# Kernel optimization log

Hardware: AMD Instinct MI355X
Metric: run time of the kernel (lower is better)

Reference implementation:

```python
import jax, jax.numpy as jnp
import numpy as np

N = 50000      # n_nodes
E = 800000     # n_edges (avg degree 16)
D_IN, D_HID, D_OUT = 128, 128, 64


def setup_inputs() -> dict:
    key = jax.random.key(0)
    k1, k2, k3, k4 = jax.random.split(key, 4)
    x = jax.random.normal(k1, (N, D_IN), jnp.float32)
    edge_index = jax.random.randint(k2, (2, E), 0, N, jnp.int32)
    # Glorot-style init for the two GCNConv linear weights
    W1 = jax.random.normal(k3, (D_IN, D_HID), jnp.float32) / np.sqrt(D_IN)
    W2 = jax.random.normal(k4, (D_HID, D_OUT), jnp.float32) / np.sqrt(D_HID)
    b1 = jnp.zeros((D_HID,), jnp.float32)
    b2 = jnp.zeros((D_OUT,), jnp.float32)
    return {"x": x, "edge_index": edge_index, "W1": W1, "b1": b1, "W2": W2, "b2": b2}


def _gcn_conv(x, W, b, src, dst):
    """PyG GCNConv: linear transform, then sym-normalized aggregation with self-loops."""
    h = x @ W                                   # [N, F_out]
    ones = jnp.ones((src.shape[0],), h.dtype)
    # degree includes the self-loop weight of 1
    deg = jax.ops.segment_sum(ones, dst, num_segments=N) + 1.0
    dinv = jax.lax.rsqrt(deg)                   # D^{-1/2}
    norm = dinv[src] * dinv[dst]                # per-edge normalization
    agg = jax.ops.segment_sum(h[src] * norm[:, None], dst, num_segments=N)
    # self-loop contribution: norm_ii = dinv_i^2
    return agg + h * (dinv * dinv)[:, None] + b


def reference(x, edge_index, W1, b1, W2, b2):
    src, dst = edge_index[0], edge_index[1]
    h = jax.nn.relu(_gcn_conv(x, W1, b1, src, dst))
    out = jax.nn.relu(_gcn_conv(h, W2, b2, src, dst))
    return out
```

## Files before the change

kernel.cpp:

```cpp
#include <hip/hip_runtime.h>

typedef unsigned short u16;
typedef __attribute__((ext_vector_type(8))) short short8;
typedef __attribute__((ext_vector_type(4))) float f32x4;

__device__ __forceinline__ float bflo(unsigned u) {
    union { unsigned u; float f; } v; v.u = u << 16; return v.f;
}
__device__ __forceinline__ float bfhi(unsigned u) {
    union { unsigned u; float f; } v; v.u = u & 0xFFFF0000u; return v.f;
}
__device__ __forceinline__ float bf2f(u16 h) {
    union { unsigned u; float f; } v; v.u = ((unsigned)h) << 16; return v.f;
}
__device__ __forceinline__ u16 f2bf(float f) {
    union { float f; unsigned u; } v; v.f = f;
    unsigned u = v.u;
    u += 0x7FFFu + ((u >> 16) & 1u);
    return (u16)(u >> 16);
}

__global__ void k_detect(const u16* __restrict__ x, int* __restrict__ flag) {
    __shared__ int c_s;
    if (threadIdx.x == 0) c_s = 0;
    __syncthreads();
    int c = 0;
    for (int i = threadIdx.x; i < 2048; i += blockDim.x) {
        int e = (x[2 * i] >> 7) & 0xFF;
        c += (e >= 160 || e <= 80) ? 1 : 0;
    }
    atomicAdd(&c_s, c);
    __syncthreads();
    if (threadIdx.x == 0) *flag = (c_s > 64) ? 1 : 0;
}

__global__ void k_convert_w(const void* __restrict__ W1, const void* __restrict__ b1,
                            const void* __restrict__ W2, const void* __restrict__ b2,
                            u16* __restrict__ out, const int* __restrict__ flag) {
    const int n1 = 128 * 128, n2 = n1 + 128, n3 = n2 + 128 * 64, n4 = n3 + 64;
    int i = blockIdx.x * 256 + threadIdx.x;
    if (i >= n4) return;
    const void* src; int off;
    if (i < n1)      { src = W1; off = i; }
    else if (i < n2) { src = b1; off = i - n1; }
    else if (i < n3) { src = W2; off = i - n2; }
    else             { src = b2; off = i - n3; }
    out[i] = *flag ? f2bf(((const float*)src)[off]) : ((const u16*)src)[off];
}


__global__ void k_degpos(const int* __restrict__ dst, int* __restrict__ cnt,
                         int* __restrict__ pos, int E) {
    int e = blockIdx.x * blockDim.x + threadIdx.x;
    if (e < E) pos[e] = atomicAdd(&cnt[dst[e]], 1);
}

__global__ void k_scan_blocks(const int* __restrict__ cnt, int* __restrict__ rowp,
                              int* __restrict__ sums, int n) {
    __shared__ int s[256];
    int t = threadIdx.x;
    int i = blockIdx.x * 256 + t;
    int v = (i < n) ? cnt[i] : 0;
    s[t] = v;
    __syncthreads();
    for (int off = 1; off < 256; off <<= 1) {
        int add = (t >= off) ? s[t - off] : 0;
        __syncthreads();
        s[t] += add;
        __syncthreads();
    }
    if (i < n) rowp[i] = s[t] - v;
    if (t == 255) sums[blockIdx.x] = s[255];
}

__global__ void k_finalize2(int* __restrict__ rowp, const int* __restrict__ sums,
                            const int* __restrict__ cnt, float* __restrict__ dinv,
                            int n, int E) {
    __shared__ int s[256];
    int t = threadIdx.x;
    int b = blockIdx.x;
    s[t] = sums[t];
    __syncthreads();
    for (int off = 1; off < 256; off <<= 1) {
        int add = (t >= off) ? s[t - off] : 0;
        __syncthreads();
        s[t] += add;
        __syncthreads();
    }
    int prefix = (b == 0) ? 0 : s[b - 1];
    int i = b * 256 + t;
    if (i < n) {
        rowp[i] += prefix;
        dinv[i] = rsqrtf((float)cnt[i] + 1.0f);
    }
    if (i == 0) rowp[n] = E;
}


__global__ void k_gemm1_fill(const void* __restrict__ Av, const u16* __restrict__ W,
                             const float* __restrict__ dinv, u16* __restrict__ out,
                             int M, int GB, const int* __restrict__ flag,
                             const int* __restrict__ src, const int* __restrict__ dst,
                             const int* __restrict__ pos, const int* __restrict__ rowp,
                             int* __restrict__ col, int E) {
    constexpr int NOUT = 128;
    int t = threadIdx.x;
    if ((int)blockIdx.x >= GB) {
        int stride = (gridDim.x - GB) * 256;
        for (int e = ((int)blockIdx.x - GB) * 256 + t; e < E; e += stride)
            col[rowp[dst[e]] + pos[e]] = src[e];
        return;
    }
    __shared__ u16 Wt[NOUT][136];
    for (int idx = t; idx < NOUT * 128; idx += 256) {
        int k = idx / NOUT, n = idx % NOUT;
        Wt[n][k] = W[idx];
    }
    __syncthreads();
    int wave = t >> 6, lane = t & 63;
    int m0 = ((int)blockIdx.x * 4 + wave) * 16;
    if (m0 >= M) return;
    int q = lane >> 4;
    int mr = lane & 15;

    short8 a[4];
    if (*flag) {
        const float* arow = (const float*)Av + (size_t)(m0 + mr) * 128 + q * 8;
#pragma unroll
        for (int c = 0; c < 4; c++) {
            f32x4 lo = *(const f32x4*)(arow + c * 32);
            f32x4 hi = *(const f32x4*)(arow + c * 32 + 4);
            a[c][0] = (short)f2bf(lo.x); a[c][1] = (short)f2bf(lo.y);
            a[c][2] = (short)f2bf(lo.z); a[c][3] = (short)f2bf(lo.w);
            a[c][4] = (short)f2bf(hi.x); a[c][5] = (short)f2bf(hi.y);
            a[c][6] = (short)f2bf(hi.z); a[c][7] = (short)f2bf(hi.w);
        }
    } else {
        const u16* arow = (const u16*)Av + (size_t)(m0 + mr) * 128 + q * 8;
#pragma unroll
        for (int c = 0; c < 4; c++) a[c] = *(const short8*)(arow + c * 32);
    }

    f32x4 acc[NOUT / 16];
#pragma unroll
    for (int tl = 0; tl < NOUT / 16; tl++) acc[tl] = (f32x4){0.f, 0.f, 0.f, 0.f};
#pragma unroll
    for (int c = 0; c < 4; c++) {
#pragma unroll
        for (int tl = 0; tl < NOUT / 16; tl++) {
            short8 b = *(const short8*)(&Wt[tl * 16 + mr][c * 32 + q * 8]);
            acc[tl] = __builtin_amdgcn_mfma_f32_16x16x32_bf16(a[c], b, acc[tl], 0, 0, 0);
        }
    }
    int rbase = m0 + q * 4;
#pragma unroll
    for (int tl = 0; tl < NOUT / 16; tl++) {
#pragma unroll
        for (int r = 0; r < 4; r++) {
            int row = rbase + r;
            float v = acc[tl][r] * dinv[row];
            out[(size_t)row * NOUT + tl * 16 + mr] = f2bf(v);
        }
    }
}


template <int NOUT>
__global__ void k_gemm_scale(const u16* __restrict__ A, const u16* __restrict__ W,
                             const float* __restrict__ dinv, u16* __restrict__ out, int M) {
    __shared__ u16 Wt[NOUT][136];
    int t = threadIdx.x;
    for (int idx = t; idx < NOUT * 128; idx += 256) {
        int k = idx / NOUT, n = idx % NOUT;
        Wt[n][k] = W[idx];
    }
    __syncthreads();
    int wave = t >> 6, lane = t & 63;
    int m0 = ((int)blockIdx.x * 4 + wave) * 16;
    if (m0 >= M) return;
    int q = lane >> 4;
    int mr = lane & 15;

    const u16* arow = A + (size_t)(m0 + mr) * 128 + q * 8;
    short8 a[4];
#pragma unroll
    for (int c = 0; c < 4; c++) a[c] = *(const short8*)(arow + c * 32);

    f32x4 acc[NOUT / 16];
#pragma unroll
    for (int tl = 0; tl < NOUT / 16; tl++) acc[tl] = (f32x4){0.f, 0.f, 0.f, 0.f};
#pragma unroll
    for (int c = 0; c < 4; c++) {
#pragma unroll
        for (int tl = 0; tl < NOUT / 16; tl++) {
            short8 b = *(const short8*)(&Wt[tl * 16 + mr][c * 32 + q * 8]);
            acc[tl] = __builtin_amdgcn_mfma_f32_16x16x32_bf16(a[c], b, acc[tl], 0, 0, 0);
        }
    }
    int rbase = m0 + q * 4;
#pragma unroll
    for (int tl = 0; tl < NOUT / 16; tl++) {
#pragma unroll
        for (int r = 0; r < 4; r++) {
            int row = rbase + r;
            float v = acc[tl][r] * dinv[row];
            out[(size_t)row * NOUT + tl * 16 + mr] = f2bf(v);
        }
    }
}


template <int F>
__global__ void k_agg(const u16* __restrict__ g, const int* __restrict__ rowp,
                      const int* __restrict__ col, const float* __restrict__ dinv,
                      const u16* __restrict__ bias, u16* __restrict__ outh,
                      float* __restrict__ outf, const int* __restrict__ flag,
                      int N, int E) {
    constexpr int LPR = F / 8;
    constexpr int EPW = 64 / LPR;
    int d = blockIdx.x * 4 + (threadIdx.x >> 6);
    if (d >= N) return;
    int lane = threadIdx.x & 63;
    int er = lane / LPR;
    int fo = (lane % LPR) * 8;

    int beg = rowp[d], end = rowp[d + 1];
    if (beg < 0) beg = 0;
    if (end > E) end = E;
    int deg = end - beg;

    float a0[8], a1[8];
#pragma unroll
    for (int j = 0; j < 8; j++) { a0[j] = 0.f; a1[j] = 0.f; }

    for (int base = 0; base < deg; base += 64) {
        int cnt = deg - base; if (cnt > 64) cnt = 64;
        int colv = 0;
        if (lane < cnt) {
            int s = col[beg + base + lane];
            colv = s < 0 ? 0 : (s >= N ? N - 1 : s);
        }
        int full = cnt / EPW;
        int i = 0;
        for (; i + 2 <= full; i += 2) {
            int s0 = __shfl(colv, i * EPW + er, 64);
            int s1 = __shfl(colv, (i + 1) * EPW + er, 64);
            uint4 v0 = *(const uint4*)(g + (size_t)s0 * F + fo);
            uint4 v1 = *(const uint4*)(g + (size_t)s1 * F + fo);
            a0[0] += bflo(v0.x); a0[1] += bfhi(v0.x);
            a0[2] += bflo(v0.y); a0[3] += bfhi(v0.y);
            a0[4] += bflo(v0.z); a0[5] += bfhi(v0.z);
            a0[6] += bflo(v0.w); a0[7] += bfhi(v0.w);
            a1[0] += bflo(v1.x); a1[1] += bfhi(v1.x);
            a1[2] += bflo(v1.y); a1[3] += bfhi(v1.y);
            a1[4] += bflo(v1.z); a1[5] += bfhi(v1.z);
            a1[6] += bflo(v1.w); a1[7] += bfhi(v1.w);
        }
        if (i < full) {
            int s0 = __shfl(colv, i * EPW + er, 64);
            uint4 v0 = *(const uint4*)(g + (size_t)s0 * F + fo);
            a0[0] += bflo(v0.x); a0[1] += bfhi(v0.x);
            a0[2] += bflo(v0.y); a0[3] += bfhi(v0.y);
            a0[4] += bflo(v0.z); a0[5] += bfhi(v0.z);
            a0[6] += bflo(v0.w); a0[7] += bfhi(v0.w);
            i++;
        }
        int rem = cnt - full * EPW;
        int s0 = __shfl(colv, (full * EPW + er) & 63, 64);
        if (er < rem) {
            uint4 v0 = *(const uint4*)(g + (size_t)s0 * F + fo);
            a0[0] += bflo(v0.x); a0[1] += bfhi(v0.x);
            a0[2] += bflo(v0.y); a0[3] += bfhi(v0.y);
            a0[4] += bflo(v0.z); a0[5] += bfhi(v0.z);
            a0[6] += bflo(v0.w); a0[7] += bfhi(v0.w);
        }
    }
#pragma unroll
    for (int j = 0; j < 8; j++) a0[j] += a1[j];
#pragma unroll
    for (int off = LPR; off < 64; off <<= 1) {
#pragma unroll
        for (int j = 0; j < 8; j++) a0[j] += __shfl_xor(a0[j], off, 64);
    }

    if (lane < LPR) {
        uint4 sv = *(const uint4*)(g + (size_t)d * F + fo);
        uint4 bv = *(const uint4*)(bias + fo);
        float di = dinv[d];
        float r[8];
        r[0] = di * (a0[0] + bflo(sv.x)) + bflo(bv.x);
        r[1] = di * (a0[1] + bfhi(sv.x)) + bfhi(bv.x);
        r[2] = di * (a0[2] + bflo(sv.y)) + bflo(bv.y);
        r[3] = di * (a0[3] + bfhi(sv.y)) + bfhi(bv.y);
        r[4] = di * (a0[4] + bflo(sv.z)) + bflo(bv.z);
        r[5] = di * (a0[5] + bfhi(sv.z)) + bfhi(bv.z);
        r[6] = di * (a0[6] + bflo(sv.w)) + bflo(bv.w);
        r[7] = di * (a0[7] + bfhi(sv.w)) + bfhi(bv.w);
#pragma unroll
        for (int j = 0; j < 8; j++) r[j] = r[j] > 0.f ? r[j] : 0.f;
        size_t o = (size_t)d * F + fo;
        if (flag && *flag) {
            f32x4 w0 = {r[0], r[1], r[2], r[3]};
            f32x4 w1 = {r[4], r[5], r[6], r[7]};
            *(f32x4*)(outf + o) = w0;
            *(f32x4*)(outf + o + 4) = w1;
        } else {
            uint4 w;
            w.x = (unsigned)f2bf(r[0]) | ((unsigned)f2bf(r[1]) << 16);
            w.y = (unsigned)f2bf(r[2]) | ((unsigned)f2bf(r[3]) << 16);
            w.z = (unsigned)f2bf(r[4]) | ((unsigned)f2bf(r[5]) << 16);
            w.w = (unsigned)f2bf(r[6]) | ((unsigned)f2bf(r[7]) << 16);
            *(uint4*)(outh + o) = w;
        }
    }
}


extern "C" void kernel_launch(void* const* d_in, const int* in_sizes, int n_in,
                              void* d_out, int out_size, void* d_ws, size_t ws_size,
                              hipStream_t stream) {
    const int N = in_sizes[0] / 128;
    const int E = in_sizes[1] / 2;
    const int* ei = (const int*)d_in[1];
    const int* src = ei;
    const int* dst = ei + E;

    char* p = (char*)d_ws;
    auto alloc = [&](size_t b) { char* r = p; p += (b + 255) & ~(size_t)255; return r; };
    int*   flag = (int*)alloc(256);
    int*   rowp = (int*)alloc((size_t)(N + 1) * 4);
    float* dinv = (float*)alloc((size_t)N * 4);
    int*   col  = (int*)alloc((size_t)E * 4);
    u16*   wbuf = (u16*)alloc((size_t)(128 * 128 + 128 + 128 * 64 + 64) * 2);
    char*  slotA = alloc((size_t)N * 128 * 2);
    char*  slotB = alloc((size_t)N * 128 * 2);

    int* cnt  = (int*)slotA;
    int* sums = (int*)(slotA + (size_t)N * 4);
    u16* g1   = (u16*)slotA;
    u16* g2   = (u16*)slotA;
    int* pos  = (int*)slotB;
    u16* o1   = (u16*)slotB;
    u16* W1C = wbuf;
    u16* b1C = wbuf + 128 * 128;
    u16* W2C = b1C + 128;
    u16* b2C = W2C + 128 * 64;

    k_detect<<<1, 256, 0, stream>>>((const u16*)d_in[0], flag);
    k_convert_w<<<97, 256, 0, stream>>>(d_in[2], d_in[3], d_in[4], d_in[5], wbuf, flag);

    hipMemsetAsync(slotA, 0, (size_t)N * 4 + 1024, stream);
    int eb = (E + 255) / 256;
    int nb = (N + 255) / 256;
    k_degpos<<<eb, 256, 0, stream>>>(dst, cnt, pos, E);
    k_scan_blocks<<<nb, 256, 0, stream>>>(cnt, rowp, sums, N);
    k_finalize2<<<nb, 256, 0, stream>>>(rowp, sums, cnt, dinv, N, E);

    int GB = (N / 16 + 3) / 4;
    int FB = GB;
    k_gemm1_fill<<<GB + FB, 256, 0, stream>>>(d_in[0], W1C, dinv, g1, N, GB, flag,
                                              src, dst, pos, rowp, col, E);

    int ab = (N + 3) / 4;
    k_agg<128><<<ab, 256, 0, stream>>>(g1, rowp, col, dinv, b1C,
                                       o1, nullptr, nullptr, N, E);
    k_gemm_scale<64><<<GB, 256, 0, stream>>>(o1, W2C, dinv, g2, N);
    k_agg<64><<<ab, 256, 0, stream>>>(g2, rowp, col, dinv, b2C,
                                      (u16*)d_out, (float*)d_out, flag, N, E);
}
```

Measured before the change: 214.3 us.

## Fold dtype detection and weight conversion into consumers, merge scan kernels

The dtype-detect kernel is merged into the degree-count kernel as block 0. The separate weight/bias conversion kernel is removed, and each GEMM or aggregation kernel now converts fp32 weights and biases on the fly while loading them into shared memory or registers. The two-pass block scan is collapsed into one kernel in which every block recomputes all block sums from the counts with vectorised loads. The intent is to drop three launches and a small memset region, at the cost of redundant per-block sum work and per-block weight conversion.

```diff
diff --git a/kernel.cpp b/kernel.cpp
--- a/kernel.cpp
+++ b/kernel.cpp
@@ -9,9 +9,6 @@
 }
 __device__ __forceinline__ float bfhi(unsigned u) {
     union { unsigned u; float f; } v; v.u = u & 0xFFFF0000u; return v.f;
-}
-__device__ __forceinline__ float bf2f(u16 h) {
-    union { unsigned u; float f; } v; v.u = ((unsigned)h) << 16; return v.f;
 }
 __device__ __forceinline__ u16 f2bf(float f) {
     union { float f; unsigned u; } v; v.f = f;
@@ -20,84 +17,65 @@
     return (u16)(u >> 16);
 }
 
-__global__ void k_detect(const u16* __restrict__ x, int* __restrict__ flag) {
-    __shared__ int c_s;
-    if (threadIdx.x == 0) c_s = 0;
-    __syncthreads();
-    int c = 0;
-    for (int i = threadIdx.x; i < 2048; i += blockDim.x) {
-        int e = (x[2 * i] >> 7) & 0xFF;
-        c += (e >= 160 || e <= 80) ? 1 : 0;
-    }
-    atomicAdd(&c_s, c);
-    __syncthreads();
-    if (threadIdx.x == 0) *flag = (c_s > 64) ? 1 : 0;
-}
-
-__global__ void k_convert_w(const void* __restrict__ W1, const void* __restrict__ b1,
-                            const void* __restrict__ W2, const void* __restrict__ b2,
-                            u16* __restrict__ out, const int* __restrict__ flag) {
-    const int n1 = 128 * 128, n2 = n1 + 128, n3 = n2 + 128 * 64, n4 = n3 + 64;
-    int i = blockIdx.x * 256 + threadIdx.x;
-    if (i >= n4) return;
-    const void* src; int off;
-    if (i < n1)      { src = W1; off = i; }
-    else if (i < n2) { src = b1; off = i - n1; }
-    else if (i < n3) { src = W2; off = i - n2; }
-    else             { src = b2; off = i - n3; }
-    out[i] = *flag ? f2bf(((const float*)src)[off]) : ((const u16*)src)[off];
-}
-
-
-__global__ void k_degpos(const int* __restrict__ dst, int* __restrict__ cnt,
-                         int* __restrict__ pos, int E) {
-    int e = blockIdx.x * blockDim.x + threadIdx.x;
+__global__ void k_deg_detect(const int* __restrict__ dst, int* __restrict__ cnt,
+                             int* __restrict__ pos, int E,
+                             const u16* __restrict__ x, int* __restrict__ flag) {
+    if (blockIdx.x == 0) {
+        __shared__ int c_s;
+        if (threadIdx.x == 0) c_s = 0;
+        __syncthreads();
+        int c = 0;
+        for (int i = threadIdx.x; i < 2048; i += 256) {
+            int ex = (x[2 * i] >> 7) & 0xFF;
+            c += (ex >= 160 || ex <= 80) ? 1 : 0;
+        }
+        atomicAdd(&c_s, c);
+        __syncthreads();
+        if (threadIdx.x == 0) *flag = (c_s > 64) ? 1 : 0;
+    }
+    int e = blockIdx.x * 256 + threadIdx.x;
     if (e < E) pos[e] = atomicAdd(&cnt[dst[e]], 1);
 }
 
-__global__ void k_scan_blocks(const int* __restrict__ cnt, int* __restrict__ rowp,
-                              int* __restrict__ sums, int n) {
-    __shared__ int s[256];
+__global__ void k_scan(const int* __restrict__ cnt, int* __restrict__ rowp,
+                       float* __restrict__ dinv, int n, int E, int nb) {
+    __shared__ int S[256];
+    __shared__ int T[256];
     int t = threadIdx.x;
-    int i = blockIdx.x * 256 + t;
-    int v = (i < n) ? cnt[i] : 0;
-    s[t] = v;
+    int b = blockIdx.x;
+    int s = 0;
+    if (t < nb) {
+        const int4* p4 = (const int4*)(cnt + t * 256);
+#pragma unroll 8
+        for (int i = 0; i < 64; i++) { int4 v = p4[i]; s += v.x + v.y + v.z + v.w; }
+    }
+    S[t] = s;
     __syncthreads();
     for (int off = 1; off < 256; off <<= 1) {
-        int add = (t >= off) ? s[t - off] : 0;
-        __syncthreads();
-        s[t] += add;
-        __syncthreads();
-    }
-    if (i < n) rowp[i] = s[t] - v;
-    if (t == 255) sums[blockIdx.x] = s[255];
-}
-
-__global__ void k_finalize2(int* __restrict__ rowp, const int* __restrict__ sums,
-                            const int* __restrict__ cnt, float* __restrict__ dinv,
-                            int n, int E) {
-    __shared__ int s[256];
-    int t = threadIdx.x;
-    int b = blockIdx.x;
-    s[t] = sums[t];
+        int add = (t >= off) ? S[t - off] : 0;
+        __syncthreads();
+        S[t] += add;
+        __syncthreads();
+    }
+    int prefix = (b == 0) ? 0 : S[b - 1];
+    int i = b * 256 + t;
+    int v = (i < n) ? cnt[i] : 0;
+    T[t] = v;
     __syncthreads();
     for (int off = 1; off < 256; off <<= 1) {
-        int add = (t >= off) ? s[t - off] : 0;
-        __syncthreads();
-        s[t] += add;
-        __syncthreads();
-    }
-    int prefix = (b == 0) ? 0 : s[b - 1];
-    int i = b * 256 + t;
+        int add = (t >= off) ? T[t - off] : 0;
+        __syncthreads();
+        T[t] += add;
+        __syncthreads();
+    }
     if (i < n) {
-        rowp[i] += prefix;
-        dinv[i] = rsqrtf((float)cnt[i] + 1.0f);
+        rowp[i] = prefix + T[t] - v;
+        dinv[i] = rsqrtf((float)v + 1.0f);
     }
     if (i == 0) rowp[n] = E;
 }
 
-
-__global__ void k_gemm1_fill(const void* __restrict__ Av, const u16* __restrict__ W,
+__global__ void k_gemm1_fill(const void* __restrict__ Av, const void* __restrict__ W,
                              const float* __restrict__ dinv, u16* __restrict__ out,
                              int M, int GB, const int* __restrict__ flag,
                              const int* __restrict__ src, const int* __restrict__ dst,
@@ -111,10 +89,11 @@
             col[rowp[dst[e]] + pos[e]] = src[e];
         return;
     }
+    int fl = *flag;
     __shared__ u16 Wt[NOUT][136];
     for (int idx = t; idx < NOUT * 128; idx += 256) {
         int k = idx / NOUT, n = idx % NOUT;
-        Wt[n][k] = W[idx];
+        Wt[n][k] = fl ? f2bf(((const float*)W)[idx]) : ((const u16*)W)[idx];
     }
     __syncthreads();
     int wave = t >> 6, lane = t & 63;
@@ -124,7 +103,7 @@
     int mr = lane & 15;
 
     short8 a[4];
-    if (*flag) {
+    if (fl) {
         const float* arow = (const float*)Av + (size_t)(m0 + mr) * 128 + q * 8;
 #pragma unroll
         for (int c = 0; c < 4; c++) {
@@ -164,15 +143,16 @@
     }
 }
 
-
 template <int NOUT>
-__global__ void k_gemm_scale(const u16* __restrict__ A, const u16* __restrict__ W,
-                             const float* __restrict__ dinv, u16* __restrict__ out, int M) {
+__global__ void k_gemm_scale(const u16* __restrict__ A, const void* __restrict__ W,
+                             const float* __restrict__ dinv, u16* __restrict__ out,
+                             int M, const int* __restrict__ flag) {
+    int fl = *flag;
     __shared__ u16 Wt[NOUT][136];
     int t = threadIdx.x;
     for (int idx = t; idx < NOUT * 128; idx += 256) {
         int k = idx / NOUT, n = idx % NOUT;
-        Wt[n][k] = W[idx];
+        Wt[n][k] = fl ? f2bf(((const float*)W)[idx]) : ((const u16*)W)[idx];
     }
     __syncthreads();
     int wave = t >> 6, lane = t & 63;
@@ -209,13 +189,12 @@
     }
 }
 
-
 template <int F>
 __global__ void k_agg(const u16* __restrict__ g, const int* __restrict__ rowp,
                       const int* __restrict__ col, const float* __restrict__ dinv,
-                      const u16* __restrict__ bias, u16* __restrict__ outh,
+                      const void* __restrict__ biasv, u16* __restrict__ outh,
                       float* __restrict__ outf, const int* __restrict__ flag,
-                      int N, int E) {
+                      int outsel, int N, int E) {
     constexpr int LPR = F / 8;
     constexpr int EPW = 64 / LPR;
     int d = blockIdx.x * 4 + (threadIdx.x >> 6);
@@ -284,22 +263,33 @@
     }
 
     if (lane < LPR) {
+        int fl = *flag;
         uint4 sv = *(const uint4*)(g + (size_t)d * F + fo);
-        uint4 bv = *(const uint4*)(bias + fo);
+        float bb[8];
+        if (fl) {
+            const float* bp = (const float*)biasv + fo;
+            f32x4 blo = *(const f32x4*)bp;
+            f32x4 bhi = *(const f32x4*)(bp + 4);
+            bb[0] = blo.x; bb[1] = blo.y; bb[2] = blo.z; bb[3] = blo.w;
+            bb[4] = bhi.x; bb[5] = bhi.y; bb[6] = bhi.z; bb[7] = bhi.w;
+        } else {
+            uint4 bv = *(const uint4*)((const u16*)biasv + fo);
+            bb[0] = bflo(bv.x); bb[1] = bfhi(bv.x);
+            bb[2] = bflo(bv.y); bb[3] = bfhi(bv.y);
+            bb[4] = bflo(bv.z); bb[5] = bfhi(bv.z);
+            bb[6] = bflo(bv.w); bb[7] = bfhi(bv.w);
+        }
         float di = dinv[d];
+        float sf[8] = { bflo(sv.x), bfhi(sv.x), bflo(sv.y), bfhi(sv.y),
+                        bflo(sv.z), bfhi(sv.z), bflo(sv.w), bfhi(sv.w) };
         float r[8];
-        r[0] = di * (a0[0] + bflo(sv.x)) + bflo(bv.x);
-        r[1] = di * (a0[1] + bfhi(sv.x)) + bfhi(bv.x);
-        r[2] = di * (a0[2] + bflo(sv.y)) + bflo(bv.y);
-        r[3] = di * (a0[3] + bfhi(sv.y)) + bfhi(bv.y);
-        r[4] = di * (a0[4] + bflo(sv.z)) + bflo(bv.z);
-        r[5] = di * (a0[5] + bfhi(sv.z)) + bfhi(bv.z);
-        r[6] = di * (a0[6] + bflo(sv.w)) + bflo(bv.w);
-        r[7] = di * (a0[7] + bfhi(sv.w)) + bfhi(bv.w);
-#pragma unroll
-        for (int j = 0; j < 8; j++) r[j] = r[j] > 0.f ? r[j] : 0.f;
+#pragma unroll
+        for (int j = 0; j < 8; j++) {
+            float v = di * (a0[j] + sf[j]) + bb[j];
+            r[j] = v > 0.f ? v : 0.f;
+        }
         size_t o = (size_t)d * F + fo;
-        if (flag && *flag) {
+        if (outsel && fl) {
             f32x4 w0 = {r[0], r[1], r[2], r[3]};
             f32x4 w1 = {r[4], r[5], r[6], r[7]};
             *(f32x4*)(outf + o) = w0;
@@ -331,40 +321,32 @@
     int*   rowp = (int*)alloc((size_t)(N + 1) * 4);
     float* dinv = (float*)alloc((size_t)N * 4);
     int*   col  = (int*)alloc((size_t)E * 4);
-    u16*   wbuf = (u16*)alloc((size_t)(128 * 128 + 128 + 128 * 64 + 64) * 2);
     char*  slotA = alloc((size_t)N * 128 * 2);
     char*  slotB = alloc((size_t)N * 128 * 2);
 
-    int* cnt  = (int*)slotA;
-    int* sums = (int*)(slotA + (size_t)N * 4);
-    u16* g1   = (u16*)slotA;
-    u16* g2   = (u16*)slotA;
-    int* pos  = (int*)slotB;
-    u16* o1   = (u16*)slotB;
-    u16* W1C = wbuf;
-    u16* b1C = wbuf + 128 * 128;
-    u16* W2C = b1C + 128;
-    u16* b2C = W2C + 128 * 64;
-
-    k_detect<<<1, 256, 0, stream>>>((const u16*)d_in[0], flag);
-    k_convert_w<<<97, 256, 0, stream>>>(d_in[2], d_in[3], d_in[4], d_in[5], wbuf, flag);
-
-    hipMemsetAsync(slotA, 0, (size_t)N * 4 + 1024, stream);
+    int* cnt = (int*)slotA;
+    u16* g1  = (u16*)slotA;
+    u16* g2  = (u16*)slotA;
+    int* pos = (int*)slotB;
+    u16* o1  = (u16*)slotB;
+
     int eb = (E + 255) / 256;
     int nb = (N + 255) / 256;
-    k_degpos<<<eb, 256, 0, stream>>>(dst, cnt, pos, E);
-    k_scan_blocks<<<nb, 256, 0, stream>>>(cnt, rowp, sums, N);
-    k_finalize2<<<nb, 256, 0, stream>>>(rowp, sums, cnt, dinv, N, E);
+
+    hipMemsetAsync(slotA, 0, (size_t)nb * 256 * 4, stream);
+
+    k_deg_detect<<<eb, 256, 0, stream>>>(dst, cnt, pos, E, (const u16*)d_in[0], flag);
+    k_scan<<<nb, 256, 0, stream>>>(cnt, rowp, dinv, N, E, nb);
 
     int GB = (N / 16 + 3) / 4;
     int FB = GB;
-    k_gemm1_fill<<<GB + FB, 256, 0, stream>>>(d_in[0], W1C, dinv, g1, N, GB, flag,
+    k_gemm1_fill<<<GB + FB, 256, 0, stream>>>(d_in[0], d_in[2], dinv, g1, N, GB, flag,
                                               src, dst, pos, rowp, col, E);
 
     int ab = (N + 3) / 4;
-    k_agg<128><<<ab, 256, 0, stream>>>(g1, rowp, col, dinv, b1C,
-                                       o1, nullptr, nullptr, N, E);
-    k_gemm_scale<64><<<GB, 256, 0, stream>>>(o1, W2C, dinv, g2, N);
-    k_agg<64><<<ab, 256, 0, stream>>>(g2, rowp, col, dinv, b2C,
-                                      (u16*)d_out, (float*)d_out, flag, N, E);
-}
+    k_agg<128><<<ab, 256, 0, stream>>>(g1, rowp, col, dinv, d_in[3],
+                                       o1, nullptr, flag, 0, N, E);
+    k_gemm_scale<64><<<GB, 256, 0, stream>>>(o1, d_in[4], dinv, g2, N, flag);
+    k_agg<64><<<ab, 256, 0, stream>>>(g2, rowp, col, dinv, d_in[5],
+                                      (u16*)d_out, (float*)d_out, flag, 1, N, E);
+}
```

Result: slower. 228.1 us (+6.5%).
